# Kernel tuning notes

Hardware: AMD Instinct MI355X
Metric: run time of the kernel (lower is better)

## Reference

```python
import jax, jax.numpy as jnp
import numpy as np

DIM = 384
HEADS = 12
WH, WW = 7, 7
N = WH * WW
NW = 64          # windows per image
B_ = 4096        # total windows (64 images * 64 windows)


def _relative_position_index():
    ch = np.arange(WH)
    cw = np.arange(WW)
    coords = np.stack(np.meshgrid(ch, cw, indexing='ij'))          # 2, Wh, Ww
    cf = coords.reshape(2, -1)                                     # 2, N
    rel = cf[:, :, None] - cf[:, None, :]                          # 2, N, N
    rel = rel.transpose(1, 2, 0).copy()                            # N, N, 2
    rel[:, :, 0] += WH - 1
    rel[:, :, 1] += WW - 1
    rel[:, :, 0] *= 2 * WW - 1
    return rel.sum(-1).astype(np.int32)                            # N, N


def setup_inputs() -> dict:
    key = jax.random.key(0)
    ks = jax.random.split(key, 7)
    x = jax.random.normal(ks[0], (B_, N, DIM), dtype=jnp.float32)
    mask = jax.random.normal(ks[1], (NW, N, N), dtype=jnp.float32)
    qkv_w = jax.random.normal(ks[2], (3 * DIM, DIM), dtype=jnp.float32) * 0.02
    qkv_b = jax.random.normal(ks[3], (3 * DIM,), dtype=jnp.float32) * 0.02
    proj_w = jax.random.normal(ks[4], (DIM, DIM), dtype=jnp.float32) * 0.02
    proj_b = jax.random.normal(ks[5], (DIM,), dtype=jnp.float32) * 0.02
    bias_table = jax.random.normal(ks[6], (169, HEADS), dtype=jnp.float32) * 0.02
    rel_idx = jnp.asarray(_relative_position_index())
    return {"x": x, "mask": mask, "qkv_w": qkv_w, "qkv_b": qkv_b,
            "proj_w": proj_w, "proj_b": proj_b, "bias_table": bias_table,
            "rel_idx": rel_idx}


def reference(x, mask, qkv_w, qkv_b, proj_w, proj_b, bias_table, rel_idx):
    B, Nn, C = x.shape
    hd = C // HEADS
    scale = hd ** (-0.5)
    # qkv projection: (B, N, 3C) -> (3, B, H, N, hd)
    qkv = (x @ qkv_w.T + qkv_b).reshape(B, Nn, 3, HEADS, hd).transpose(2, 0, 3, 1, 4)
    q, k, v = qkv[0], qkv[1], qkv[2]
    attn = jnp.einsum('bhnd,bhmd->bhnm', q * scale, k)             # B, H, N, N
    # gathered relative-position bias: (N, N, H) -> (H, N, N)
    bias = bias_table[rel_idx.reshape(-1)].reshape(Nn, Nn, HEADS).transpose(2, 0, 1)
    attn = attn + bias[None]
    nW = mask.shape[0]
    attn = attn.reshape(B // nW, nW, HEADS, Nn, Nn) + mask[None, :, None]
    attn = attn.reshape(B, HEADS, Nn, Nn)
    attn = jax.nn.softmax(attn, axis=-1)
    out = jnp.einsum('bhnm,bhmd->bnhd', attn, v).reshape(B, Nn, C)
    return out @ proj_w.T + proj_b
```

## Files before the change

### kernel.cpp

```cpp
#include <hip/hip_runtime.h>


#define NTOK 49
#define DIM 384
#define HEADS 12
#define QKV_OC 1152
#define QKV_ELEMS (1152*384)
#define PROJ_ELEMS (384*384)
#define CMB_ELEMS (64*12*49*49)
#define SCALE 0.17677669529663687f

typedef __attribute__((ext_vector_type(8))) __bf16 bf16x8;
typedef __attribute__((ext_vector_type(4))) float f32x4;

union BF8 { bf16x8 v; unsigned short u[8]; uint4 q; };

#define GLOAD_LDS16(gp, lp)                                                  \
  __builtin_amdgcn_global_load_lds(                                          \
      (const __attribute__((address_space(1))) void*)(gp),                   \
      (__attribute__((address_space(3))) void*)(lp), 16, 0, 0)

__device__ __forceinline__ unsigned short f2bf(float f) {
  union { float f; unsigned u; } x; x.f = f;
  unsigned r = x.u + 0x7fffu + ((x.u >> 16) & 1u);
  return (unsigned short)(r >> 16);
}

__device__ __forceinline__ bf16x8 zbf8() {
  BF8 z;
  #pragma unroll
  for (int j = 0; j < 8; ++j) z.u[j] = 0;
  return z.v;
}

__global__ void prep_kernel(const float* __restrict__ qkv_w,
                            const float* __restrict__ proj_w,
                            const float* __restrict__ bias_table,
                            const int* __restrict__ rel_idx,
                            const float* __restrict__ mask,
                            const float* __restrict__ qkv_b,
                            unsigned short* __restrict__ wq,
                            unsigned short* __restrict__ wp,
                            float* __restrict__ cmb,
                            float* __restrict__ qb2) {
  int i = blockIdx.x * 256 + threadIdx.x;
  if (i < QKV_ELEMS) {
    int c = i / 384, j = i % 384, s = j >> 3, e = j & 7;
    float v = qkv_w[c * 384 + ((s ^ (c & 7)) << 3) + e];
    if (c < 384) v *= SCALE;
    wq[i] = f2bf(v);
  } else if (i < QKV_ELEMS + PROJ_ELEMS) {
    int k = i - QKV_ELEMS;
    int c = k / 384, j = k % 384, s = j >> 3, e = j & 7;
    wp[k] = f2bf(proj_w[c * 384 + ((s ^ (c & 7)) << 3) + e]);
  } else if (i < QKV_ELEMS + PROJ_ELEMS + CMB_ELEMS) {
    int j = i - QKV_ELEMS - PROJ_ELEMS;
    int row = j % 49;
    int tok = (j / 49) % 49;
    int h   = (j / 2401) % 12;
    int wi  = j / (2401 * 12);
    cmb[j] = bias_table[rel_idx[row * 49 + tok] * HEADS + h]
           + mask[(wi * 49 + row) * 49 + tok];
  } else if (i < QKV_ELEMS + PROJ_ELEMS + CMB_ELEMS + QKV_OC) {
    int c = i - QKV_ELEMS - PROJ_ELEMS - CMB_ELEMS;
    qb2[c] = qkv_b[c] * (c < 384 ? SCALE : 1.0f);
  }
}

template<int NS, int FP32IN, int BF16OUT>
__global__ __launch_bounds__(256, 6) void gemm_lds(
    const void* __restrict__ Ain, const unsigned short* __restrict__ Wsw,
    const float* __restrict__ bias, void* __restrict__ Cout, int Mrows) {
  __shared__ alignas(16) unsigned short Bsm[32 * 384];
  const int tid = threadIdx.x;
  const int wave = tid >> 6, lane = tid & 63, g = lane >> 4, li = lane & 15;
  const int tb = blockIdx.x * 64 + wave * 16;
  const int arow = tb + li;

  bf16x8 afr[12];
  if (arow < Mrows) {
    if (FP32IN) {
      const float* ap = (const float*)Ain + (size_t)arow * 384 + g * 8;
      #pragma unroll
      for (int ks = 0; ks < 12; ++ks) {
        float4 f0 = *(const float4*)(ap + ks * 32);
        float4 f1 = *(const float4*)(ap + ks * 32 + 4);
        BF8 t;
        t.u[0] = f2bf(f0.x); t.u[1] = f2bf(f0.y); t.u[2] = f2bf(f0.z); t.u[3] = f2bf(f0.w);
        t.u[4] = f2bf(f1.x); t.u[5] = f2bf(f1.y); t.u[6] = f2bf(f1.z); t.u[7] = f2bf(f1.w);
        afr[ks] = t.v;
      }
    } else {
      const unsigned short* ap = (const unsigned short*)Ain + (size_t)arow * 384 + g * 8;
      #pragma unroll
      for (int ks = 0; ks < 12; ++ks) afr[ks] = *(const bf16x8*)(ap + ks * 32);
    }
  } else {
    bf16x8 z = zbf8();
    #pragma unroll
    for (int ks = 0; ks < 12; ++ks) afr[ks] = z;
  }

  #pragma unroll 1
  for (int ns = 0; ns < NS; ++ns) {
    {
      const unsigned short* gs = Wsw + (size_t)ns * 12288 + wave * 3072 + lane * 8;
      unsigned short* ls = &Bsm[wave * 3072];
      #pragma unroll
      for (int i = 0; i < 6; ++i) GLOAD_LDS16(gs + i * 512, ls + i * 512);
    }
    __syncthreads();

    f32x4 acc[2];
    acc[0] = (f32x4){0.f, 0.f, 0.f, 0.f};
    acc[1] = (f32x4){0.f, 0.f, 0.f, 0.f};
    #pragma unroll
    for (int k2 = 0; k2 < 12; ++k2) {
      #pragma unroll
      for (int nt = 0; nt < 2; ++nt) {
        bf16x8 bf = *(const bf16x8*)&Bsm[(nt * 16 + li) * 384 +
                                         (((k2 * 4 + g) ^ (li & 7)) << 3)];
        acc[nt] = __builtin_amdgcn_mfma_f32_16x16x32_bf16(afr[k2], bf, acc[nt], 0, 0, 0);
      }
    }

    #pragma unroll
    for (int nt = 0; nt < 2; ++nt) {
      int col = ns * 32 + nt * 16 + li;
      float bv = bias[col];
      #pragma unroll
      for (int r4 = 0; r4 < 4; ++r4) {
        int row = tb + g * 4 + r4;
        if (row < Mrows) {
          float v = acc[nt][r4] + bv;
          if (BF16OUT) ((unsigned short*)Cout)[(size_t)row * (NS * 32) + col] = f2bf(v);
          else         ((float*)Cout)[(size_t)row * (NS * 32) + col] = v;
        }
      }
    }
    __syncthreads();
  }
}

#define AT_K 0
#define AT_V (49*128)
#define AT_ELEMS (AT_V + 49*138)

__global__ __launch_bounds__(512, 6) void attn_kernel(
    const unsigned short* __restrict__ qkv,
    const float* __restrict__ cmb,
    unsigned short* __restrict__ Obuf,
    int wb0) {
  __shared__ unsigned short lds[AT_ELEMS];
  const int tid  = threadIdx.x;
  const int wave = tid >> 6, lane = tid & 63;
  const int g = lane >> 4, li = lane & 15;
  const int relw = blockIdx.x;
  const int wi = (wb0 + relw) & 63;
  const size_t rowbase = (size_t)relw * 49;
  const int mgrp = wave >> 1, ng = wave & 1;
  const int arow = mgrp * 16 + li;

  #pragma unroll 1
  for (int c = 0; c < 3; ++c) {
    if (c) __syncthreads();
    #pragma unroll
    for (int it = 0; it < 2; ++it) {
      int gidx = it * 512 + tid;
      if (gidx < 784) {
        int row = gidx >> 4, gc = gidx & 15;
        bf16x8 v = *(const bf16x8*)(qkv + (rowbase + row) * 1152 + 384 + c * 128 + gc * 8);
        *(bf16x8*)&lds[AT_K + row * 128 + ((gc ^ (row & 7)) << 3)] = v;
      }
    }
    #pragma unroll
    for (int it = 0; it < 2; ++it) {
      int gidx = it * 512 + tid;
      if (gidx < 784) {
        int row = gidx >> 4, gc = gidx & 15;
        BF8 v;
        v.q = *(const uint4*)(qkv + (rowbase + row) * 1152 + 768 + c * 128 + gc * 8);
        int e = AT_V + row * 138 + gc * 8;
        *(unsigned*)&lds[e]     = v.q.x;
        *(unsigned*)&lds[e + 2] = v.q.y;
        *(unsigned*)&lds[e + 4] = v.q.z;
        *(unsigned*)&lds[e + 6] = v.q.w;
      }
    }
    __syncthreads();

    #pragma unroll 1
    for (int b = 0; b < 2; ++b) {
      const int hh = ng * 2 + b;
      const int h  = c * 4 + hh;

      bf16x8 qa = (arow < NTOK)
          ? *(const bf16x8*)(qkv + (rowbase + arow) * 1152 + h * 32 + g * 8)
          : zbf8();

      f32x4 sv[4];
      #pragma unroll
      for (int nt = 0; nt < 4; ++nt) {
        int tok = nt * 16 + li;
        bf16x8 kf = (tok < NTOK)
            ? *(const bf16x8*)&lds[AT_K + tok * 128 + (((hh * 4 + g) ^ (tok & 7)) << 3)]
            : zbf8();
        f32x4 z4 = (f32x4){0.f, 0.f, 0.f, 0.f};
        sv[nt] = __builtin_amdgcn_mfma_f32_16x16x32_bf16(kf, qa, z4, 0, 0, 0);
      }

      const float* cb = cmb + (size_t)(wi * HEADS + h) * (NTOK * NTOK);
      #pragma unroll
      for (int nt = 0; nt < 4; ++nt) {
        #pragma unroll
        for (int r4 = 0; r4 < 4; ++r4) {
          int tok = nt * 16 + g * 4 + r4;
          float v;
          if (tok < NTOK) {
            v = sv[nt][r4];
            if (arow < NTOK) v += cb[tok * NTOK + arow];
          } else {
            v = -1e30f;
          }
          sv[nt][r4] = v;
        }
      }

      float m = -1e30f;
      #pragma unroll
      for (int nt = 0; nt < 4; ++nt)
        #pragma unroll
        for (int r4 = 0; r4 < 4; ++r4) m = fmaxf(m, sv[nt][r4]);
      m = fmaxf(m, __shfl_xor(m, 16));
      m = fmaxf(m, __shfl_xor(m, 32));
      float s = 0.f;
      #pragma unroll
      for (int nt = 0; nt < 4; ++nt)
        #pragma unroll
        for (int r4 = 0; r4 < 4; ++r4) {
          float e = __expf(sv[nt][r4] - m);
          sv[nt][r4] = e;
          s += e;
        }
      s += __shfl_xor(s, 16);
      s += __shfl_xor(s, 32);
      float inv = 1.f / s;
      #pragma unroll
      for (int nt = 0; nt < 4; ++nt)
        #pragma unroll
        for (int r4 = 0; r4 < 4; ++r4) sv[nt][r4] *= inv;

      bf16x8 pa[2];
      #pragma unroll
      for (int k2 = 0; k2 < 2; ++k2) {
        BF8 pf;
        #pragma unroll
        for (int j = 0; j < 8; ++j) {
          int srcLane = (((g * 2 + (j >> 2)) & 3) << 4) | li;
          float v0 = __shfl(sv[k2 * 2][j & 3], srcLane);
          float v1 = __shfl(sv[k2 * 2 + 1][j & 3], srcLane);
          pf.u[j] = f2bf((g >= 2) ? v1 : v0);
        }
        pa[k2] = pf.v;
      }

      f32x4 oa[2];
      oa[0] = (f32x4){0.f, 0.f, 0.f, 0.f};
      oa[1] = (f32x4){0.f, 0.f, 0.f, 0.f};
      #pragma unroll
      for (int k2 = 0; k2 < 2; ++k2) {
        #pragma unroll
        for (int nt2 = 0; nt2 < 2; ++nt2) {
          BF8 vb;
          int ch = hh * 32 + nt2 * 16 + li;
          #pragma unroll
          for (int j = 0; j < 8; ++j) {
            int tok = k2 * 32 + g * 8 + j;
            vb.u[j] = (tok < NTOK) ? lds[AT_V + tok * 138 + ch] : (unsigned short)0;
          }
          oa[nt2] = __builtin_amdgcn_mfma_f32_16x16x32_bf16(pa[k2], vb.v, oa[nt2], 0, 0, 0);
        }
      }

      #pragma unroll
      for (int nt2 = 0; nt2 < 2; ++nt2) {
        int col = h * 32 + nt2 * 16 + li;
        #pragma unroll
        for (int r4 = 0; r4 < 4; ++r4) {
          int row = mgrp * 16 + g * 4 + r4;
          if (row < NTOK)
            Obuf[(rowbase + row) * 384 + col] = f2bf(oa[nt2][r4]);
        }
      }
    }
  }
}

extern "C" void kernel_launch(void* const* d_in, const int* in_sizes, int n_in,
                              void* d_out, int out_size, void* d_ws, size_t ws_size,
                              hipStream_t stream) {
  (void)in_sizes; (void)n_in; (void)out_size;
  const float* x          = (const float*)d_in[0];
  const float* mask       = (const float*)d_in[1];
  const float* qkv_w      = (const float*)d_in[2];
  const float* qkv_b      = (const float*)d_in[3];
  const float* proj_w     = (const float*)d_in[4];
  const float* proj_b     = (const float*)d_in[5];
  const float* bias_table = (const float*)d_in[6];
  const int*   rel_idx    = (const int*)d_in[7];
  float* out = (float*)d_out;

  char* ws = (char*)d_ws;
  size_t off = 0;
  unsigned short* wq  = (unsigned short*)(ws + off); off += (size_t)QKV_ELEMS * 2;
  unsigned short* wp  = (unsigned short*)(ws + off); off += (size_t)PROJ_ELEMS * 2;
  float*          qb2 = (float*)(ws + off);          off += (size_t)QKV_OC * 4;
  float*          cmb = (float*)(ws + off);          off += (size_t)CMB_ELEMS * 4;
  const size_t fixed = off;

  const int cands[7] = {2048, 4096, 1024, 512, 256, 128, 64};
  int WB = 64;
  for (int ci = 0; ci < 7; ++ci) {
    size_t need = fixed + (size_t)cands[ci] * 49 * (1152 + 384) * 2;
    if (need <= ws_size) { WB = cands[ci]; break; }
  }
  unsigned short* qkv = (unsigned short*)(ws + fixed);
  unsigned short* xb  = qkv + (size_t)WB * 49 * 1152;

  const int prep_total = QKV_ELEMS + PROJ_ELEMS + CMB_ELEMS + QKV_OC;
  prep_kernel<<<(prep_total + 255) / 256, 256, 0, stream>>>(
      qkv_w, proj_w, bias_table, rel_idx, mask, qkv_b, wq, wp, cmb, qb2);

  const int NB = 4096 / WB;
  const int Mrows = WB * 49;
  const int grid = (Mrows + 63) / 64;
  for (int b = 0; b < NB; ++b) {
    gemm_lds<36, 1, 1><<<grid, 256, 0, stream>>>(
        (const void*)(x + (size_t)b * Mrows * 384), wq, qb2, (void*)qkv, Mrows);
    attn_kernel<<<WB, 512, 0, stream>>>(qkv, cmb, xb, b * WB);
    gemm_lds<12, 0, 0><<<grid, 256, 0, stream>>>(
        (const void*)xb, wp, proj_b, (void*)(out + (size_t)b * Mrows * 384), Mrows);
  }
}
```

Measured before the change: 1.023 ms.

## Replace row-panel GEMMs with 128x128 LDS-tiled GEMM and pre-swizzled bf16 activations

```diff
diff --git a/kernel.cpp b/kernel.cpp
--- a/kernel.cpp
+++ b/kernel.cpp
@@ -67,78 +67,108 @@
   }
 }
 
-template<int NS, int FP32IN, int BF16OUT>
-__global__ __launch_bounds__(256, 6) void gemm_lds(
-    const void* __restrict__ Ain, const unsigned short* __restrict__ Wsw,
-    const float* __restrict__ bias, void* __restrict__ Cout, int Mrows) {
-  __shared__ alignas(16) unsigned short Bsm[32 * 384];
+__global__ void convx_kernel(const float* __restrict__ x,
+                             unsigned short* __restrict__ xsw, long ngran) {
+  long gidx = (long)blockIdx.x * 256 + threadIdx.x;
+  if (gidx >= ngran) return;
+  int r = (int)(gidx / 48), s = (int)(gidx % 48);
+  int ssrc = (s & 56) | ((s & 7) ^ (r & 7));
+  const float* src = x + (size_t)r * 384 + ssrc * 8;
+  float4 f0 = *(const float4*)src;
+  float4 f1 = *(const float4*)(src + 4);
+  BF8 t;
+  t.u[0] = f2bf(f0.x); t.u[1] = f2bf(f0.y); t.u[2] = f2bf(f0.z); t.u[3] = f2bf(f0.w);
+  t.u[4] = f2bf(f1.x); t.u[5] = f2bf(f1.y); t.u[6] = f2bf(f1.z); t.u[7] = f2bf(f1.w);
+  *(uint4*)(xsw + (size_t)r * 384 + s * 8) = t.q;
+}
+
+template<int BF16OUT>
+__global__ __launch_bounds__(256, 4) void gemm128(
+    const unsigned short* __restrict__ Asw, const unsigned short* __restrict__ Wsw,
+    const float* __restrict__ bias, void* __restrict__ Cout,
+    int Mrows, int Ntot, int NRB) {
+  __shared__ alignas(16) unsigned short As[128 * 64];
+  __shared__ alignas(16) unsigned short Bs[128 * 64];
+  const int bid = blockIdx.x;
+  const int rowb = bid % NRB, colp = bid / NRB;
+  const int tb = rowb * 128, nb = colp * 128;
   const int tid = threadIdx.x;
   const int wave = tid >> 6, lane = tid & 63, g = lane >> 4, li = lane & 15;
-  const int tb = blockIdx.x * 64 + wave * 16;
-  const int arow = tb + li;
-
-  bf16x8 afr[12];
-  if (arow < Mrows) {
-    if (FP32IN) {
-      const float* ap = (const float*)Ain + (size_t)arow * 384 + g * 8;
-      #pragma unroll
-      for (int ks = 0; ks < 12; ++ks) {
-        float4 f0 = *(const float4*)(ap + ks * 32);
-        float4 f1 = *(const float4*)(ap + ks * 32 + 4);
-        BF8 t;
-        t.u[0] = f2bf(f0.x); t.u[1] = f2bf(f0.y); t.u[2] = f2bf(f0.z); t.u[3] = f2bf(f0.w);
-        t.u[4] = f2bf(f1.x); t.u[5] = f2bf(f1.y); t.u[6] = f2bf(f1.z); t.u[7] = f2bf(f1.w);
-        afr[ks] = t.v;
-      }
-    } else {
-      const unsigned short* ap = (const unsigned short*)Ain + (size_t)arow * 384 + g * 8;
-      #pragma unroll
-      for (int ks = 0; ks < 12; ++ks) afr[ks] = *(const bf16x8*)(ap + ks * 32);
-    }
-  } else {
-    bf16x8 z = zbf8();
-    #pragma unroll
-    for (int ks = 0; ks < 12; ++ks) afr[ks] = z;
-  }
+  const int wr = wave >> 1, wc = wave & 1;
+  const int chbase = wave * 256 + lane;
+
+  f32x4 acc[4][4];
+  #pragma unroll
+  for (int m = 0; m < 4; ++m)
+    #pragma unroll
+    for (int n = 0; n < 4; ++n) acc[m][n] = (f32x4){0.f, 0.f, 0.f, 0.f};
 
   #pragma unroll 1
-  for (int ns = 0; ns < NS; ++ns) {
-    {
-      const unsigned short* gs = Wsw + (size_t)ns * 12288 + wave * 3072 + lane * 8;
-      unsigned short* ls = &Bsm[wave * 3072];
-      #pragma unroll
-      for (int i = 0; i < 6; ++i) GLOAD_LDS16(gs + i * 512, ls + i * 512);
+  for (int step = 0; step < 6; ++step) {
+    const int k0 = step * 64;
+    if (step) __syncthreads();
+    #pragma unroll
+    for (int i = 0; i < 4; ++i) {
+      int ch = chbase + i * 64;
+      int r = ch >> 3, s = ch & 7;
+      GLOAD_LDS16(Asw + (size_t)(tb + r) * 384 + k0 + s * 8,
+                  (unsigned short*)As + ch * 8);
+    }
+    #pragma unroll
+    for (int i = 0; i < 4; ++i) {
+      int ch = chbase + i * 64;
+      int c = ch >> 3, s = ch & 7;
+      GLOAD_LDS16(Wsw + (size_t)(nb + c) * 384 + k0 + s * 8,
+                  (unsigned short*)Bs + ch * 8);
     }
     __syncthreads();
 
-    f32x4 acc[2];
-    acc[0] = (f32x4){0.f, 0.f, 0.f, 0.f};
-    acc[1] = (f32x4){0.f, 0.f, 0.f, 0.f};
-    #pragma unroll
-    for (int k2 = 0; k2 < 12; ++k2) {
-      #pragma unroll
-      for (int nt = 0; nt < 2; ++nt) {
-        bf16x8 bf = *(const bf16x8*)&Bsm[(nt * 16 + li) * 384 +
-                                         (((k2 * 4 + g) ^ (li & 7)) << 3)];
-        acc[nt] = __builtin_amdgcn_mfma_f32_16x16x32_bf16(afr[k2], bf, acc[nt], 0, 0, 0);
-      }
-    }
-
-    #pragma unroll
-    for (int nt = 0; nt < 2; ++nt) {
-      int col = ns * 32 + nt * 16 + li;
-      float bv = bias[col];
+    #pragma unroll
+    for (int kk = 0; kk < 2; ++kk) {
+      const int goff = ((kk * 4 + g) ^ (li & 7)) << 3;
+      bf16x8 a0 = *(const bf16x8*)&As[(wr * 64 +  0 + li) * 64 + goff];
+      bf16x8 a1 = *(const bf16x8*)&As[(wr * 64 + 16 + li) * 64 + goff];
+      bf16x8 a2 = *(const bf16x8*)&As[(wr * 64 + 32 + li) * 64 + goff];
+      bf16x8 a3 = *(const bf16x8*)&As[(wr * 64 + 48 + li) * 64 + goff];
+      bf16x8 b0 = *(const bf16x8*)&Bs[(wc * 64 +  0 + li) * 64 + goff];
+      bf16x8 b1 = *(const bf16x8*)&Bs[(wc * 64 + 16 + li) * 64 + goff];
+      bf16x8 b2 = *(const bf16x8*)&Bs[(wc * 64 + 32 + li) * 64 + goff];
+      bf16x8 b3 = *(const bf16x8*)&Bs[(wc * 64 + 48 + li) * 64 + goff];
+      acc[0][0] = __builtin_amdgcn_mfma_f32_16x16x32_bf16(a0, b0, acc[0][0], 0, 0, 0);
+      acc[0][1] = __builtin_amdgcn_mfma_f32_16x16x32_bf16(a0, b1, acc[0][1], 0, 0, 0);
+      acc[0][2] = __builtin_amdgcn_mfma_f32_16x16x32_bf16(a0, b2, acc[0][2], 0, 0, 0);
+      acc[0][3] = __builtin_amdgcn_mfma_f32_16x16x32_bf16(a0, b3, acc[0][3], 0, 0, 0);
+      acc[1][0] = __builtin_amdgcn_mfma_f32_16x16x32_bf16(a1, b0, acc[1][0], 0, 0, 0);
+      acc[1][1] = __builtin_amdgcn_mfma_f32_16x16x32_bf16(a1, b1, acc[1][1], 0, 0, 0);
+      acc[1][2] = __builtin_amdgcn_mfma_f32_16x16x32_bf16(a1, b2, acc[1][2], 0, 0, 0);
+      acc[1][3] = __builtin_amdgcn_mfma_f32_16x16x32_bf16(a1, b3, acc[1][3], 0, 0, 0);
+      acc[2][0] = __builtin_amdgcn_mfma_f32_16x16x32_bf16(a2, b0, acc[2][0], 0, 0, 0);
+      acc[2][1] = __builtin_amdgcn_mfma_f32_16x16x32_bf16(a2, b1, acc[2][1], 0, 0, 0);
+      acc[2][2] = __builtin_amdgcn_mfma_f32_16x16x32_bf16(a2, b2, acc[2][2], 0, 0, 0);
+      acc[2][3] = __builtin_amdgcn_mfma_f32_16x16x32_bf16(a2, b3, acc[2][3], 0, 0, 0);
+      acc[3][0] = __builtin_amdgcn_mfma_f32_16x16x32_bf16(a3, b0, acc[3][0], 0, 0, 0);
+      acc[3][1] = __builtin_amdgcn_mfma_f32_16x16x32_bf16(a3, b1, acc[3][1], 0, 0, 0);
+      acc[3][2] = __builtin_amdgcn_mfma_f32_16x16x32_bf16(a3, b2, acc[3][2], 0, 0, 0);
+      acc[3][3] = __builtin_amdgcn_mfma_f32_16x16x32_bf16(a3, b3, acc[3][3], 0, 0, 0);
+    }
+  }
+
+  #pragma unroll
+  for (int n = 0; n < 4; ++n) {
+    int col = nb + wc * 64 + n * 16 + li;
+    float bv = bias[col];
+    #pragma unroll
+    for (int m = 0; m < 4; ++m) {
       #pragma unroll
       for (int r4 = 0; r4 < 4; ++r4) {
-        int row = tb + g * 4 + r4;
+        int row = tb + wr * 64 + m * 16 + g * 4 + r4;
         if (row < Mrows) {
-          float v = acc[nt][r4] + bv;
-          if (BF16OUT) ((unsigned short*)Cout)[(size_t)row * (NS * 32) + col] = f2bf(v);
-          else         ((float*)Cout)[(size_t)row * (NS * 32) + col] = v;
-        }
-      }
-    }
-    __syncthreads();
+          float v = acc[m][n][r4] + bv;
+          if (BF16OUT) ((unsigned short*)Cout)[(size_t)row * Ntot + col] = f2bf(v);
+          else         ((float*)Cout)[(size_t)row * Ntot + col] = v;
+        }
+      }
+    }
   }
 }
 
@@ -284,12 +314,16 @@
 
       #pragma unroll
       for (int nt2 = 0; nt2 < 2; ++nt2) {
-        int col = h * 32 + nt2 * 16 + li;
+        int colb = h * 32 + nt2 * 16 + li;
+        int gran = colb >> 3;
         #pragma unroll
         for (int r4 = 0; r4 < 4; ++r4) {
           int row = mgrp * 16 + g * 4 + r4;
-          if (row < NTOK)
-            Obuf[(rowbase + row) * 384 + col] = f2bf(oa[nt2][r4]);
+          if (row < NTOK) {
+            int grow = (int)(rowbase) + row;
+            int col2 = (((gran & 56) | ((gran & 7) ^ (grow & 7))) << 3) | (colb & 7);
+            Obuf[(size_t)grow * 384 + col2] = f2bf(oa[nt2][r4]);
+          }
         }
       }
     }
@@ -321,24 +355,30 @@
   const int cands[7] = {2048, 4096, 1024, 512, 256, 128, 64};
   int WB = 64;
   for (int ci = 0; ci < 7; ++ci) {
-    size_t need = fixed + (size_t)cands[ci] * 49 * (1152 + 384) * 2;
+    int mrows = cands[ci] * 49;
+    int mpad = ((mrows + 127) / 128) * 128;
+    size_t need = fixed + (size_t)mpad * 384 * 2 + (size_t)mrows * 1152 * 2;
     if (need <= ws_size) { WB = cands[ci]; break; }
   }
-  unsigned short* qkv = (unsigned short*)(ws + fixed);
-  unsigned short* xb  = qkv + (size_t)WB * 49 * 1152;
+  const int Mrows = WB * 49;
+  const int Mpad  = ((Mrows + 127) / 128) * 128;
+  const int NRB   = Mpad / 128;
+  unsigned short* xsw = (unsigned short*)(ws + fixed);
+  unsigned short* qkv = xsw + (size_t)Mpad * 384;
 
   const int prep_total = QKV_ELEMS + PROJ_ELEMS + CMB_ELEMS + QKV_OC;
   prep_kernel<<<(prep_total + 255) / 256, 256, 0, stream>>>(
       qkv_w, proj_w, bias_table, rel_idx, mask, qkv_b, wq, wp, cmb, qb2);
 
   const int NB = 4096 / WB;
-  const int Mrows = WB * 49;
-  const int grid = (Mrows + 63) / 64;
+  const long ngran = (long)Mrows * 48;
   for (int b = 0; b < NB; ++b) {
-    gemm_lds<36, 1, 1><<<grid, 256, 0, stream>>>(
-        (const void*)(x + (size_t)b * Mrows * 384), wq, qb2, (void*)qkv, Mrows);
-    attn_kernel<<<WB, 512, 0, stream>>>(qkv, cmb, xb, b * WB);
-    gemm_lds<12, 0, 0><<<grid, 256, 0, stream>>>(
-        (const void*)xb, wp, proj_b, (void*)(out + (size_t)b * Mrows * 384), Mrows);
-  }
-}
+    convx_kernel<<<(int)((ngran + 255) / 256), 256, 0, stream>>>(
+        x + (size_t)b * Mrows * 384, xsw, ngran);
+    gemm128<1><<<NRB * 9, 256, 0, stream>>>(xsw, wq, qb2, (void*)qkv,
+                                            Mrows, 1152, NRB);
+    attn_kernel<<<WB, 512, 0, stream>>>(qkv, cmb, xsw, b * WB);
+    gemm128<0><<<NRB * 3, 256, 0, stream>>>(xsw, wp, proj_b,
+        (void*)(out + (size_t)b * Mrows * 384), Mrows, 384, NRB);
+  }
+}
```

Measured after the change: 1.064 ms. +3.9%, slower.
